# Performance work log

Hardware: AMD Instinct MI355X
Metric: run time of the kernel (lower is better)

## Reference

```python
import jax, jax.numpy as jnp
import numpy as np

B, C, W, F, NC = 512, 12, 4, 512, 4  # batch, leads, windows(=4, hardcoded by conv0), features, classes


def setup_inputs() -> dict:
    key = jax.random.key(0)
    ks = jax.random.split(key, 16)
    g = lambda i, shape, s=1.0: jax.random.normal(ks[i], shape, jnp.float32) * s
    return {
        "x": g(0, (B, C, W, F)),
        # GRU (PyTorch layout: W_ih [3F,F], W_hh [3F,F], gate order r,z,n)
        "gru_wih": g(1, (3 * F, F), 0.03),
        "gru_whh": g(2, (3 * F, F), 0.03),
        "gru_bih": jnp.zeros((3 * F,), jnp.float32),
        "gru_bhh": jnp.zeros((3 * F,), jnp.float32),
        # GraphLearning 1x1 convs (squeezed kernels); positive biases keep adj nondegenerate
        "conv0_w": g(3, (W,), 0.5), "conv0_b": jnp.float32(0.1),
        "conv1_w": g(4, (F,), 0.05), "conv1_b": jnp.float32(0.1),
        "conv2_w": g(5, (C * C, C), 0.3),
        "conv2_b": 0.1 + 0.05 * jnp.abs(g(6, (C * C,))),
        # GCN stack
        "gcn_w": g(7, (2, F, F), 0.04), "gcn_b": jnp.zeros((2, F), jnp.float32),
        # classifier head (jax [in,out] layout); BN in eval mode
        "fc1_w": g(8, (C * F, 512), 0.02), "fc1_b": jnp.zeros((512,), jnp.float32),
        "bn1_g": jnp.ones((512,), jnp.float32), "bn1_b": jnp.zeros((512,), jnp.float32),
        "bn1_m": 0.1 * g(9, (512,)), "bn1_v": 1.0 + 0.1 * jnp.abs(g(10, (512,))),
        "fc2_w": g(11, (512, 512), 0.04), "fc2_b": jnp.zeros((512,), jnp.float32),
        "bn2_g": jnp.ones((512,), jnp.float32), "bn2_b": jnp.zeros((512,), jnp.float32),
        "bn2_m": 0.1 * g(12, (512,)), "bn2_v": 1.0 + 0.1 * jnp.abs(g(13, (512,))),
        "fc3_w": g(14, (512, NC), 0.04), "fc3_b": jnp.zeros((NC,), jnp.float32),
    }


def reference(x, gru_wih, gru_whh, gru_bih, gru_bhh,
              conv0_w, conv0_b, conv1_w, conv1_b, conv2_w, conv2_b,
              gcn_w, gcn_b,
              fc1_w, fc1_b, bn1_g, bn1_b, bn1_m, bn1_v,
              fc2_w, fc2_b, bn2_g, bn2_b, bn2_m, bn2_v,
              fc3_w, fc3_b):
    b, c, w, f = x.shape
    # --- GRU over leads dim; each window slice starts from h0=0, so merge (batch, w) ---
    xs = x.transpose(0, 2, 1, 3).reshape(b * w, c, f)            # [N, C, F]
    xW = jnp.einsum('ntf,gf->ntg', xs, gru_wih) + gru_bih        # precompute input gates [N,C,3F]

    def step(h, xw_t):
        hg = h @ gru_whh.T + gru_bhh
        xr, xz, xn = jnp.split(xw_t, 3, axis=-1)
        hr, hz, hn = jnp.split(hg, 3, axis=-1)
        r = jax.nn.sigmoid(xr + hr)
        z = jax.nn.sigmoid(xz + hz)
        n = jnp.tanh(xn + r * hn)
        h = (1.0 - z) * n + z * h
        return h, h

    _, hs = jax.lax.scan(step, jnp.zeros((b * w, f), x.dtype), xW.transpose(1, 0, 2))
    gru_out = hs.transpose(1, 0, 2).reshape(b, w, c, f).transpose(0, 2, 1, 3)  # [B,C,W,F]

    # --- GraphLearning: 1x1 convs -> 12x12 adjacency -> normalized Laplacian -> Chebyshev K=4 ---
    g0 = gru_out.transpose(0, 2, 1, 3)                               # [B,W,C,F]
    y = jax.nn.relu(jnp.einsum('bwcf,w->bcf', g0, conv0_w) + conv0_b)  # [B,C,F]
    y = jax.nn.relu(jnp.einsum('bcf,f->bc', y, conv1_w) + conv1_b)     # [B,C]
    y = jax.nn.relu(jnp.einsum('bc,kc->bk', y, conv2_w) + conv2_b)     # [B,C*C]
    a = jnp.mean(y.reshape(b, c, c), axis=0)
    adj = jax.nn.relu(a)
    degree = jnp.sum(adj, axis=1)
    adj_s = 0.5 * (adj + adj.T)
    d_hat = 1.0 / (jnp.sqrt(degree) + 1e-7)
    lap = d_hat[:, None] * (jnp.diag(degree) - adj_s) * d_hat[None, :]
    L0 = jnp.zeros_like(lap)
    L1 = lap
    L2 = 2.0 * lap @ L1 - L0
    L3 = 2.0 * lap @ L2 - L1
    cheb = jnp.stack([L0, L1, L2, L3], axis=0)                       # [4,C,C]

    # --- GCN stack with residuals (dropout is identity in eval) ---
    h = gru_out.transpose(0, 2, 1, 3)[:, :, None]                    # [B,W,1,C,F]
    tmp = h
    res = h
    for i in range(gcn_w.shape[0]):
        support = jnp.einsum('bwocf,fg->bwocg', h, gcn_w[i])
        out = jnp.einsum('wij,bwojf->bwoif', cheb, support) + gcn_b[i]
        h = jax.nn.relu(out) + res
        res = h
    h = tmp + h
    h = h[:, :, 0].sum(1).reshape(b, c * f)                          # [B, C*F]

    # --- classifier head (eval-mode BN, dropout identity) ---
    def bn(v, gmm, bt, m, var):
        return (v - m) / jnp.sqrt(var + 1e-5) * gmm + bt

    h = bn(jax.nn.leaky_relu(h @ fc1_w + fc1_b, 0.01), bn1_g, bn1_b, bn1_m, bn1_v)
    h = bn(jax.nn.leaky_relu(h @ fc2_w + fc2_b, 0.01), bn2_g, bn2_b, bn2_m, bn2_v)
    return h @ fc3_w + fc3_b
```

## Files before the change

kernel.cpp:

```cpp
#include <hip/hip_runtime.h>
#include <cmath>

constexpr int Bb  = 512;
constexpr int Cc  = 12;
constexpr int Ww  = 4;
constexpr int Ff  = 512;
constexpr int Nn  = Bb * Ww;
constexpr int Gg  = 3 * Ff;
constexpr int Mx  = Nn * Cc;

typedef __attribute__((ext_vector_type(8))) short bf16x8;
typedef __attribute__((ext_vector_type(4))) float f32x4;

__device__ __forceinline__ float sigm(float v) { return 1.f / (1.f + expf(-v)); }
__device__ __forceinline__ float b2f(ushort u) { union { float f; unsigned i; } v; v.i = ((unsigned)u) << 16; return v.f; }
__device__ __forceinline__ ushort f2b(float f) {
    union { float f; unsigned i; } v; v.f = f;
    unsigned r = v.i + 0x7FFFu + ((v.i >> 16) & 1u);
    return (ushort)(r >> 16);
}
__device__ __forceinline__ void async16(const ushort* g, ushort* l) {
    __builtin_amdgcn_global_load_lds(
        (const __attribute__((address_space(1))) unsigned int*)g,
        (__attribute__((address_space(3))) unsigned int*)l, 16, 0, 0);
}

__global__ __launch_bounds__(256) void mfma_gemm(
    const ushort* __restrict__ A, const ushort* __restrict__ Bt,
    float* __restrict__ Cf, ushort* __restrict__ Cb,
    const float* __restrict__ colBias,
    int N, int K, int kLen, int MN, int gridY)
{
    __shared__ ushort As[128 * 64], Bs[128 * 64];
    const int tid = threadIdx.x;
    const int ln = tid & 63, wv = tid >> 6;
    const int l = blockIdx.x;
    const int by = l % gridY, bx = l / gridY, bz = blockIdx.y;
    const int srow = ln >> 3;
    const int kslot = (ln & 7) ^ srow;
    const int rowA0 = by * 128 + wv * 32;
    const int rowB0 = bx * 128 + wv * 32;
    const ushort* ga = A  + (long)(rowA0 + srow) * K + bz * kLen + kslot * 8;
    const ushort* gb = Bt + (long)(rowB0 + srow) * K + bz * kLen + kslot * 8;
    ushort* la = As + wv * 32 * 64;
    ushort* lb = Bs + wv * 32 * 64;
    const int rbase = (wv >> 1) * 64, cbase = (wv & 1) * 64;
    const int mrow = ln & 15, quad = ln >> 4;

    f32x4 acc[4][4] = {};

    for (int kc = 0; kc < kLen; kc += 64) {
        #pragma unroll
        for (int i = 0; i < 4; ++i) {
            async16(ga + (long)(i * 8) * K, la + i * 8 * 64);
            async16(gb + (long)(i * 8) * K, lb + i * 8 * 64);
        }
        ga += 64; gb += 64;
        __syncthreads();
        #pragma unroll
        for (int s = 0; s < 2; ++s) {
            const int sw = (((s << 2) + quad) ^ (ln & 7)) << 3;
            bf16x8 af[4], bf[4];
            #pragma unroll
            for (int i = 0; i < 4; ++i)
                af[i] = *(const bf16x8*)(As + (rbase + i * 16 + mrow) * 64 + sw);
            #pragma unroll
            for (int j = 0; j < 4; ++j)
                bf[j] = *(const bf16x8*)(Bs + (cbase + j * 16 + mrow) * 64 + sw);
            #pragma unroll
            for (int i = 0; i < 4; ++i)
                #pragma unroll
                for (int j = 0; j < 4; ++j)
                    acc[i][j] = __builtin_amdgcn_mfma_f32_16x16x32_bf16(bf[j], af[i], acc[i][j], 0, 0, 0);
        }
        __syncthreads();
    }

    const int gr0 = by * 128 + rbase + mrow;
    const int gc0 = bx * 128 + cbase + quad * 4;
    if (Cb) {
        #pragma unroll
        for (int i = 0; i < 4; ++i) {
            const long rowoff = (long)(gr0 + i * 16) * N;
            #pragma unroll
            for (int j = 0; j < 4; ++j) {
                float c0 = 0.f, c1 = 0.f, c2 = 0.f, c3 = 0.f;
                if (colBias) {
                    const float4 cb4 = *(const float4*)(colBias + gc0 + j * 16);
                    c0 = cb4.x; c1 = cb4.y; c2 = cb4.z; c3 = cb4.w;
                }
                union { ushort u[4]; uint2 v; } pk;
                pk.u[0] = f2b(acc[i][j][0] + c0);
                pk.u[1] = f2b(acc[i][j][1] + c1);
                pk.u[2] = f2b(acc[i][j][2] + c2);
                pk.u[3] = f2b(acc[i][j][3] + c3);
                *(uint2*)&Cb[rowoff + gc0 + j * 16] = pk.v;
            }
        }
    } else {
        float* Co = Cf + (long)bz * MN;
        #pragma unroll
        for (int i = 0; i < 4; ++i) {
            const long rowoff = (long)(gr0 + i * 16) * N;
            #pragma unroll
            for (int j = 0; j < 4; ++j)
                *(f32x4*)&Co[rowoff + gc0 + j * 16] = acc[i][j];
        }
    }
}

__global__ __launch_bounds__(256) void gru_fused(
    const ushort* __restrict__ hin, const ushort* __restrict__ xb,
    const ushort* __restrict__ whhB, const ushort* __restrict__ wihB,
    const float* __restrict__ bih, const float* __restrict__ bhh,
    ushort* __restrict__ hout, ushort* __restrict__ G, int t)
{
    __shared__ ushort Ah[64 * 64], Ax[64 * 64], Bh[96 * 64], Bx[96 * 64];
    const int tid = threadIdx.x, ln = tid & 63, wv = tid >> 6;
    const int mb = blockIdx.x & 31, fb = blockIdx.x >> 5;
    const int srow = ln >> 3, kslot = (ln & 7) ^ srow;
    const int mrow = ln & 15, quad = ln >> 4;
    f32x4 aH[6] = {}, aX[6] = {};
    const ushort* hrow = hin + (long)(mb * 64) * 512;

    for (int kc = 0; kc < 512; kc += 64) {
        #pragma unroll
        for (int a = 0; a < 2; ++a) {
            const int r0 = (wv * 2 + a) * 8;
            async16(hrow + (long)(r0 + srow) * 512 + kc + kslot * 8, Ah + r0 * 64);
            async16(xb + ((long)(mb * 64 + r0 + srow) * 12 + t) * 512 + kc + kslot * 8, Ax + r0 * 64);
        }
        #pragma unroll
        for (int b8 = 0; b8 < 3; ++b8) {
            const int lr0 = (wv * 3 + b8) * 8;
            const int lr = lr0 + srow;
            const int g = lr >> 5, fc = lr & 31;
            const long wr = (long)(g * 512 + fb * 32 + fc) * 512 + kc + kslot * 8;
            async16(whhB + wr, Bh + lr0 * 64);
            async16(wihB + wr, Bx + lr0 * 64);
        }
        __syncthreads();
        #pragma unroll
        for (int s = 0; s < 2; ++s) {
            const int sw = (((s << 2) + quad) ^ (ln & 7)) << 3;
            const bf16x8 ah = *(const bf16x8*)(Ah + (wv * 16 + mrow) * 64 + sw);
            const bf16x8 ax = *(const bf16x8*)(Ax + (wv * 16 + mrow) * 64 + sw);
            #pragma unroll
            for (int jt = 0; jt < 6; ++jt) {
                const bf16x8 bh = *(const bf16x8*)(Bh + (jt * 16 + mrow) * 64 + sw);
                aH[jt] = __builtin_amdgcn_mfma_f32_16x16x32_bf16(bh, ah, aH[jt], 0, 0, 0);
            }
            #pragma unroll
            for (int jt = 0; jt < 6; ++jt) {
                const bf16x8 bx2 = *(const bf16x8*)(Bx + (jt * 16 + mrow) * 64 + sw);
                aX[jt] = __builtin_amdgcn_mfma_f32_16x16x32_bf16(bx2, ax, aX[jt], 0, 0, 0);
            }
        }
        __syncthreads();
    }

    const int n = mb * 64 + wv * 16 + mrow;
    #pragma unroll
    for (int ft = 0; ft < 2; ++ft) {
        const int f0 = fb * 32 + ft * 16 + quad * 4;
        const float4 bir = *(const float4*)(bih + f0);
        const float4 biz = *(const float4*)(bih + 512 + f0);
        const float4 bin = *(const float4*)(bih + 1024 + f0);
        const float4 bhr = *(const float4*)(bhh + f0);
        const float4 bhz = *(const float4*)(bhh + 512 + f0);
        const float4 bhn = *(const float4*)(bhh + 1024 + f0);
        union { ushort u[4]; uint2 v; } hp;
        hp.v = *(const uint2*)(hin + (long)n * 512 + f0);
        const float br[4] = {bir.x + bhr.x, bir.y + bhr.y, bir.z + bhr.z, bir.w + bhr.w};
        const float bz[4] = {biz.x + bhz.x, biz.y + bhz.y, biz.z + bhz.z, biz.w + bhz.w};
        const float bn_i[4] = {bin.x, bin.y, bin.z, bin.w};
        const float bn_h[4] = {bhn.x, bhn.y, bhn.z, bhn.w};
        union { ushort u[4]; uint2 v; } o;
        #pragma unroll
        for (int r = 0; r < 4; ++r) {
            const float rr = sigm(aH[ft][r] + aX[ft][r] + br[r]);
            const float zz = sigm(aH[2 + ft][r] + aX[2 + ft][r] + bz[r]);
            const float nv = tanhf(aX[4 + ft][r] + bn_i[r] + rr * (aH[4 + ft][r] + bn_h[r]));
            o.u[r] = f2b((1.f - zz) * nv + zz * b2f(hp.u[r]));
        }
        *(uint2*)&hout[(long)n * 512 + f0] = o.v;
        *(uint2*)&G[(long)(n * 12 + t) * 512 + f0] = o.v;
    }
}

__global__ __launch_bounds__(256) void cvt_x(const float* __restrict__ x, ushort* __restrict__ xb)
{
    const int idx = blockIdx.x * 256 + threadIdx.x;
    const int m = idx >> 6, f8 = (idx & 63) << 3;
    const int n = m / 12, c = m - n * 12;
    const int b = n >> 2, w = n & 3;
    const float* src = x + (((b * 12 + c) * 4 + w) << 9) + f8;
    const float4 a = *(const float4*)src, q = *(const float4*)(src + 4);
    uint4 o;
    o.x = (unsigned)f2b(a.x) | ((unsigned)f2b(a.y) << 16);
    o.y = (unsigned)f2b(a.z) | ((unsigned)f2b(a.w) << 16);
    o.z = (unsigned)f2b(q.x) | ((unsigned)f2b(q.y) << 16);
    o.w = (unsigned)f2b(q.z) | ((unsigned)f2b(q.w) << 16);
    *(uint4*)(xb + (m << 9) + f8) = o;
}

__global__ __launch_bounds__(256) void cvt_w2(
    const float* __restrict__ wih, const float* __restrict__ whh,
    ushort* __restrict__ wihB, ushort* __restrict__ whhB)
{
    int bx = blockIdx.x;
    const float* s; ushort* d;
    if (bx < 384) { s = wih; d = wihB; } else { s = whh; d = whhB; bx -= 384; }
    const int e = (bx * 256 + threadIdx.x) << 3;
    const float4 a = *(const float4*)(s + e), q = *(const float4*)(s + e + 4);
    uint4 o;
    o.x = (unsigned)f2b(a.x) | ((unsigned)f2b(a.y) << 16);
    o.y = (unsigned)f2b(a.z) | ((unsigned)f2b(a.w) << 16);
    o.z = (unsigned)f2b(q.x) | ((unsigned)f2b(q.y) << 16);
    o.w = (unsigned)f2b(q.z) | ((unsigned)f2b(q.w) << 16);
    *(uint4*)(d + e) = o;
}

__global__ __launch_bounds__(256) void tcvt_all(
    const float* __restrict__ gcnw, const float* __restrict__ f1w, const float* __restrict__ f2w,
    ushort* __restrict__ gw0, ushort* __restrict__ gw1,
    ushort* __restrict__ f1t, ushort* __restrict__ f2t)
{
    int by = blockIdx.y;
    const float* src; ushort* dst; int R, C;
    if (by < 16)       { src = gcnw;          dst = gw0; R = 512;  C = 512; }
    else if (by < 32)  { src = gcnw + 262144; dst = gw1; R = 512;  C = 512; by -= 16; }
    else if (by < 224) { src = f1w;           dst = f1t; R = 6144; C = 512; by -= 32; }
    else               { src = f2w;           dst = f2t; R = 512;  C = 512; by -= 224; }
    __shared__ float tl[32][33];
    const int c0 = blockIdx.x * 32, r0 = by * 32;
    const int cx = threadIdx.x & 31, ry = threadIdx.x >> 5;
    #pragma unroll
    for (int k = 0; k < 4; ++k) tl[ry + k * 8][cx] = src[(long)(r0 + ry + k * 8) * C + c0 + cx];
    __syncthreads();
    #pragma unroll
    for (int k = 0; k < 4; ++k) dst[(long)(c0 + ry + k * 8) * R + r0 + cx] = f2b(tl[cx][ry + k * 8]);
}

__global__ __launch_bounds__(256) void conv01(
    const ushort* __restrict__ G, const float* __restrict__ w0, const float* __restrict__ b0,
    const float* __restrict__ w1, const float* __restrict__ b1, float* __restrict__ y2)
{
    const int row = (blockIdx.x * 256 + threadIdx.x) >> 6;
    const int lane = threadIdx.x & 63;
    const int b = row / 12, c = row - 12 * b;
    const float w00 = w0[0], w01 = w0[1], w02 = w0[2], w03 = w0[3], bb = b0[0];
    const ushort* gp = G + ((long)(b * 4) * 12 + c) * 512;
    float s = 0.f;
    for (int f = lane; f < 512; f += 64) {
        const float v = bb + b2f(gp[f]) * w00 + b2f(gp[6144 + f]) * w01
                      + b2f(gp[12288 + f]) * w02 + b2f(gp[18432 + f]) * w03;
        s += fmaxf(v, 0.f) * w1[f];
    }
    #pragma unroll
    for (int off = 32; off; off >>= 1) s += __shfl_down(s, off);
    if (lane == 0) y2[row] = fmaxf(s + b1[0], 0.f);
}

__global__ __launch_bounds__(256) void conv2_cheb(
    const float* __restrict__ y2, const float* __restrict__ w2,
    const float* __restrict__ b2, float* __restrict__ cheb)
{
    __shared__ float ys[6144];
    __shared__ float adj[144], deg[12], dhat[12], lap[144], T2[144];
    const int tid = threadIdx.x;
    for (int i = tid; i < 6144; i += 256) ys[i] = y2[i];
    __syncthreads();
    if (tid < 144) {
        float wk[12];
        #pragma unroll
        for (int c = 0; c < 12; ++c) wk[c] = w2[tid * 12 + c];
        const float bias = b2[tid];
        float s = 0.f;
        for (int b = 0; b < 512; ++b) {
            float v = bias;
            #pragma unroll
            for (int c = 0; c < 12; ++c) v += ys[b * 12 + c] * wk[c];
            s += fmaxf(v, 0.f);
        }
        adj[tid] = fmaxf(s * (1.f / 512.f), 0.f);
    }
    __syncthreads();
    if (tid < 12) {
        float s = 0.f;
        for (int j = 0; j < 12; ++j) s += adj[tid * 12 + j];
        deg[tid] = s; dhat[tid] = 1.f / (sqrtf(s) + 1e-7f);
    }
    __syncthreads();
    if (tid < 144) {
        const int i = tid / 12, j = tid % 12;
        const float as = 0.5f * (adj[i * 12 + j] + adj[j * 12 + i]);
        lap[tid] = dhat[i] * ((i == j ? deg[i] : 0.f) - as) * dhat[j];
    }
    __syncthreads();
    if (tid < 144) {
        const int i = tid / 12, j = tid % 12;
        float s = 0.f;
        for (int kk = 0; kk < 12; ++kk) s += lap[i * 12 + kk] * lap[kk * 12 + j];
        T2[tid] = 2.f * s;
    }
    __syncthreads();
    if (tid < 144) {
        const int i = tid / 12, j = tid % 12;
        float s = 0.f;
        for (int kk = 0; kk < 12; ++kk) s += lap[i * 12 + kk] * T2[kk * 12 + j];
        cheb[tid] = 0.f;
        cheb[144 + tid] = lap[tid];
        cheb[288 + tid] = T2[tid];
        cheb[432 + tid] = 2.f * s - lap[tid];
    }
}

__global__ __launch_bounds__(256) void gcn_epi1(
    const ushort* __restrict__ S, const float* __restrict__ cheb,
    const float* __restrict__ gcnb, const ushort* __restrict__ G,
    ushort* __restrict__ H1)
{
    __shared__ float ch[576];
    const int tid = threadIdx.x;
    for (int i = tid; i < 576; i += 256) ch[i] = cheb[i];
    __syncthreads();
    const int idx = blockIdx.x * 256 + tid;
    const int f = idx & 511, bc = idx >> 9;
    const int b = bc / 12, c = bc - 12 * b;
    const float bias = gcnb[f];
    #pragma unroll
    for (int w = 0; w < 4; ++w) {
        float o = bias;
        const ushort* Sr = S + ((b * 4 + w) * 12) * 512 + f;
        const float* cw = ch + w * 144 + c * 12;
        #pragma unroll
        for (int j = 0; j < 12; ++j) o += cw[j] * b2f(Sr[j * 512]);
        const int gi = ((b * 4 + w) * 12 + c) * 512 + f;
        H1[gi] = f2b(fmaxf(o, 0.f) + b2f(G[gi]));
    }
}

__global__ __launch_bounds__(256) void gcn_epi2(
    const ushort* __restrict__ S, const float* __restrict__ cheb,
    const float* __restrict__ gcnb, const ushort* __restrict__ G,
    const ushort* __restrict__ H1, ushort* __restrict__ pooled)
{
    __shared__ float ch[576];
    const int tid = threadIdx.x;
    for (int i = tid; i < 576; i += 256) ch[i] = cheb[i];
    __syncthreads();
    const int idx = blockIdx.x * 256 + tid;
    const int f = idx & 511, bc = idx >> 9;
    const int b = bc / 12, c = bc - 12 * b;
    const float bias = gcnb[f];
    float acc = 0.f;
    #pragma unroll
    for (int w = 0; w < 4; ++w) {
        float o = bias;
        const ushort* Sr = S + ((b * 4 + w) * 12) * 512 + f;
        const float* cw = ch + w * 144 + c * 12;
        #pragma unroll
        for (int j = 0; j < 12; ++j) o += cw[j] * b2f(Sr[j * 512]);
        const int gi = ((b * 4 + w) * 12 + c) * 512 + f;
        acc += fmaxf(o, 0.f) + b2f(H1[gi]) + b2f(G[gi]);
    }
    pooled[idx] = f2b(acc);
}

__global__ __launch_bounds__(256) void fc_epi(
    const float* __restrict__ part, int nsplit, const float* __restrict__ bias,
    const float* __restrict__ g, const float* __restrict__ be,
    const float* __restrict__ mu, const float* __restrict__ var,
    ushort* __restrict__ outb, float* __restrict__ outf)
{
    const int idx = blockIdx.x * 256 + threadIdx.x;
    const int c = idx & 511;
    float s = bias[c];
    for (int k = 0; k < nsplit; ++k) s += part[k * 262144 + idx];
    s = s >= 0.f ? s : 0.01f * s;
    s = (s - mu[c]) * rsqrtf(var[c] + 1e-5f) * g[c] + be[c];
    if (outb) outb[idx] = f2b(s); else outf[idx] = s;
}

__global__ __launch_bounds__(256) void fc3_kernel(
    const float* __restrict__ z2, const float* __restrict__ w3,
    const float* __restrict__ b3, float* __restrict__ out)
{
    const int idx = blockIdx.x * 256 + threadIdx.x;
    const int m = idx >> 2, nc = idx & 3;
    float s = b3[nc];
    const float* zr = z2 + m * 512;
    for (int k = 0; k < 512; ++k) s += zr[k] * w3[k * 4 + nc];
    out[idx] = s;
}

extern "C" void kernel_launch(void* const* d_in, const int* in_sizes, int n_in,
                              void* d_out, int out_size, void* d_ws, size_t ws_size,
                              hipStream_t stream)
{
    (void)in_sizes; (void)n_in; (void)out_size; (void)ws_size;
    const float* x    = (const float*)d_in[0];
    const float* wih  = (const float*)d_in[1];
    const float* whh  = (const float*)d_in[2];
    const float* bih  = (const float*)d_in[3];
    const float* bhh  = (const float*)d_in[4];
    const float* c0w  = (const float*)d_in[5];
    const float* c0b  = (const float*)d_in[6];
    const float* c1w  = (const float*)d_in[7];
    const float* c1b  = (const float*)d_in[8];
    const float* c2w  = (const float*)d_in[9];
    const float* c2b  = (const float*)d_in[10];
    const float* gcnw = (const float*)d_in[11];
    const float* gcnb = (const float*)d_in[12];
    const float* f1w  = (const float*)d_in[13];
    const float* f1b  = (const float*)d_in[14];
    const float* bn1g = (const float*)d_in[15];
    const float* bn1b = (const float*)d_in[16];
    const float* bn1m = (const float*)d_in[17];
    const float* bn1v = (const float*)d_in[18];
    const float* f2w  = (const float*)d_in[19];
    const float* f2b_ = (const float*)d_in[20];
    const float* bn2g = (const float*)d_in[21];
    const float* bn2b = (const float*)d_in[22];
    const float* bn2m = (const float*)d_in[23];
    const float* bn2v = (const float*)d_in[24];
    const float* f3w  = (const float*)d_in[25];
    const float* f3b  = (const float*)d_in[26];

    char* W = (char*)d_ws;
    ushort* xb     = (ushort*)(W + 0);
    ushort* pooled = (ushort*)(W + 0);
    float*  z1p    = (float*)(W + 8388608);
    float*  z2p    = z1p;
    ushort* G      = (ushort*)(W + 25165824);
    ushort* S      = (ushort*)(W + 50331648);
    ushort* H1     = (ushort*)(W + 75497472);
    ushort* h0     = (ushort*)(W + 100663296);
    ushort* h1     = (ushort*)(W + 102760448);
    ushort* wihB   = (ushort*)(W + 104857600);
    ushort* whhB   = (ushort*)(W + 106430464);
    ushort* gw0    = (ushort*)(W + 108003328);
    ushort* gw1    = (ushort*)(W + 108527616);
    ushort* f1t    = (ushort*)(W + 109051904);
    ushort* f2t    = (ushort*)(W + 115343360);
    ushort* z1b    = (ushort*)(W + 115867648);
    float*  z2     = (float*)(W + 116391936);
    float*  y2     = (float*)(W + 117440512);
    float*  chebb  = (float*)(W + 117465088);

    hipMemsetAsync(h0, 0, (size_t)Nn * Ff * sizeof(ushort), stream);
    cvt_x<<<(Mx * 64) / 256, 256, 0, stream>>>(x, xb);
    cvt_w2<<<768, 256, 0, stream>>>(wih, whh, wihB, whhB);
    tcvt_all<<<dim3(16, 240), 256, 0, stream>>>(gcnw, f1w, f2w, gw0, gw1, f1t, f2t);

    ushort* hp = h0; ushort* hq = h1;
    for (int t = 0; t < Cc; ++t) {
        gru_fused<<<512, 256, 0, stream>>>(hp, xb, whhB, wihB, bih, bhh, hq, G, t);
        ushort* tmp = hp; hp = hq; hq = tmp;
    }

    conv01<<<(Bb * Cc * 64) / 256, 256, 0, stream>>>(G, c0w, c0b, c1w, c1b, y2);
    conv2_cheb<<<1, 256, 0, stream>>>(y2, c2w, c2b, chebb);

    mfma_gemm<<<dim3(768, 1), 256, 0, stream>>>(
        G, gw0, nullptr, S, nullptr, Ff, Ff, Ff, 0, 192);
    gcn_epi1<<<(Bb * Cc * Ff) / 256, 256, 0, stream>>>(S, chebb, gcnb, G, H1);

    mfma_gemm<<<dim3(768, 1), 256, 0, stream>>>(
        H1, gw1, nullptr, S, nullptr, Ff, Ff, Ff, 0, 192);
    gcn_epi2<<<(Bb * Cc * Ff) / 256, 256, 0, stream>>>(S, chebb, gcnb + Ff, G, H1, pooled);

    mfma_gemm<<<dim3(16, 16), 256, 0, stream>>>(
        pooled, f1t, z1p, nullptr, nullptr, 512, Cc * Ff, 384, 262144, 4);
    fc_epi<<<1024, 256, 0, stream>>>(z1p, 16, f1b, bn1g, bn1b, bn1m, bn1v, z1b, nullptr);
    mfma_gemm<<<dim3(16, 4), 256, 0, stream>>>(
        z1b, f2t, z2p, nullptr, nullptr, 512, 512, 128, 262144, 4);
    fc_epi<<<1024, 256, 0, stream>>>(z2p, 4, f2b_, bn2g, bn2b, bn2m, bn2v, nullptr, z2);
    fc3_kernel<<<(Bb * 4) / 256, 256, 0, stream>>>(z2, f3w, f3b, (float*)d_out);
}
```

Before: 510.4 us.

## Precompute GRU input gates in one GEMM and run recurrence as persistent kernel

Replaces the twelve per-step GRU launches with one large GEMM that precomputes the input projections for all leads, followed by a persistent kernel. That kernel keeps its slice of W_hh resident in LDS and loops over the time steps, synchronising through per-row-group atomic barriers in global memory. It also skips the recurrent matmul at t=0 and double-buffers the hidden-state loads. This removes launch overhead and the repeated W_ih/W_hh reloads per step. The cost is a spin barrier that assumes all 256 blocks are resident at once, and a bf16 round-trip on the precomputed input gates.

```diff
diff --git a/kernel.cpp b/kernel.cpp
--- a/kernel.cpp
+++ b/kernel.cpp
@@ -5,9 +5,7 @@
 constexpr int Cc  = 12;
 constexpr int Ww  = 4;
 constexpr int Ff  = 512;
-constexpr int Nn  = Bb * Ww;
-constexpr int Gg  = 3 * Ff;
-constexpr int Mx  = Nn * Cc;
+constexpr int Mx  = Bb * Ww * Cc;
 
 typedef __attribute__((ext_vector_type(8))) short bf16x8;
 typedef __attribute__((ext_vector_type(4))) float f32x4;
@@ -109,57 +107,30 @@
     }
 }
 
-__global__ __launch_bounds__(256) void gru_fused(
-    const ushort* __restrict__ hin, const ushort* __restrict__ xb,
-    const ushort* __restrict__ whhB, const ushort* __restrict__ wihB,
+__global__ __launch_bounds__(512, 1) void gru_persist(
+    const ushort* __restrict__ xW, const ushort* __restrict__ whhB,
     const float* __restrict__ bih, const float* __restrict__ bhh,
-    ushort* __restrict__ hout, ushort* __restrict__ G, int t)
-{
-    __shared__ ushort Ah[64 * 64], Ax[64 * 64], Bh[96 * 64], Bx[96 * 64];
+    ushort* __restrict__ h0, ushort* __restrict__ h1,
+    ushort* __restrict__ G, unsigned* __restrict__ bar)
+{
+    __shared__ ushort Bw[8 * 96 * 64];
+    __shared__ ushort Ah[2][128 * 64];
     const int tid = threadIdx.x, ln = tid & 63, wv = tid >> 6;
-    const int mb = blockIdx.x & 31, fb = blockIdx.x >> 5;
+    const int mb = blockIdx.x & 15, fb = blockIdx.x >> 4;
     const int srow = ln >> 3, kslot = (ln & 7) ^ srow;
     const int mrow = ln & 15, quad = ln >> 4;
-    f32x4 aH[6] = {}, aX[6] = {};
-    const ushort* hrow = hin + (long)(mb * 64) * 512;
-
-    for (int kc = 0; kc < 512; kc += 64) {
-        #pragma unroll
-        for (int a = 0; a < 2; ++a) {
-            const int r0 = (wv * 2 + a) * 8;
-            async16(hrow + (long)(r0 + srow) * 512 + kc + kslot * 8, Ah + r0 * 64);
-            async16(xb + ((long)(mb * 64 + r0 + srow) * 12 + t) * 512 + kc + kslot * 8, Ax + r0 * 64);
-        }
-        #pragma unroll
-        for (int b8 = 0; b8 < 3; ++b8) {
-            const int lr0 = (wv * 3 + b8) * 8;
-            const int lr = lr0 + srow;
-            const int g = lr >> 5, fc = lr & 31;
-            const long wr = (long)(g * 512 + fb * 32 + fc) * 512 + kc + kslot * 8;
-            async16(whhB + wr, Bh + lr0 * 64);
-            async16(wihB + wr, Bx + lr0 * 64);
-        }
-        __syncthreads();
-        #pragma unroll
-        for (int s = 0; s < 2; ++s) {
-            const int sw = (((s << 2) + quad) ^ (ln & 7)) << 3;
-            const bf16x8 ah = *(const bf16x8*)(Ah + (wv * 16 + mrow) * 64 + sw);
-            const bf16x8 ax = *(const bf16x8*)(Ax + (wv * 16 + mrow) * 64 + sw);
-            #pragma unroll
-            for (int jt = 0; jt < 6; ++jt) {
-                const bf16x8 bh = *(const bf16x8*)(Bh + (jt * 16 + mrow) * 64 + sw);
-                aH[jt] = __builtin_amdgcn_mfma_f32_16x16x32_bf16(bh, ah, aH[jt], 0, 0, 0);
-            }
-            #pragma unroll
-            for (int jt = 0; jt < 6; ++jt) {
-                const bf16x8 bx2 = *(const bf16x8*)(Bx + (jt * 16 + mrow) * 64 + sw);
-                aX[jt] = __builtin_amdgcn_mfma_f32_16x16x32_bf16(bx2, ax, aX[jt], 0, 0, 0);
-            }
-        }
-        __syncthreads();
-    }
-
-    const int n = mb * 64 + wv * 16 + mrow;
+
+    #pragma unroll
+    for (int i = 0; i < 12; ++i) {
+        const int rg = i * 8 + wv;
+        const int kc6 = rg / 12, rgi = rg - kc6 * 12;
+        const int r0 = rgi * 8, r = r0 + srow;
+        const int g = r >> 5, fc = r & 31;
+        async16(whhB + (long)(g * 512 + fb * 32 + fc) * 512 + kc6 * 64 + kslot * 8,
+                Bw + (kc6 * 96 + r0) * 64);
+    }
+
+    float br[2][4], bz[2][4], bni[2][4], bnh[2][4];
     #pragma unroll
     for (int ft = 0; ft < 2; ++ft) {
         const int f0 = fb * 32 + ft * 16 + quad * 4;
@@ -169,22 +140,98 @@
         const float4 bhr = *(const float4*)(bhh + f0);
         const float4 bhz = *(const float4*)(bhh + 512 + f0);
         const float4 bhn = *(const float4*)(bhh + 1024 + f0);
-        union { ushort u[4]; uint2 v; } hp;
-        hp.v = *(const uint2*)(hin + (long)n * 512 + f0);
-        const float br[4] = {bir.x + bhr.x, bir.y + bhr.y, bir.z + bhr.z, bir.w + bhr.w};
-        const float bz[4] = {biz.x + bhz.x, biz.y + bhz.y, biz.z + bhz.z, biz.w + bhz.w};
-        const float bn_i[4] = {bin.x, bin.y, bin.z, bin.w};
-        const float bn_h[4] = {bhn.x, bhn.y, bhn.z, bhn.w};
-        union { ushort u[4]; uint2 v; } o;
-        #pragma unroll
-        for (int r = 0; r < 4; ++r) {
-            const float rr = sigm(aH[ft][r] + aX[ft][r] + br[r]);
-            const float zz = sigm(aH[2 + ft][r] + aX[2 + ft][r] + bz[r]);
-            const float nv = tanhf(aX[4 + ft][r] + bn_i[r] + rr * (aH[4 + ft][r] + bn_h[r]));
-            o.u[r] = f2b((1.f - zz) * nv + zz * b2f(hp.u[r]));
-        }
-        *(uint2*)&hout[(long)n * 512 + f0] = o.v;
-        *(uint2*)&G[(long)(n * 12 + t) * 512 + f0] = o.v;
+        br[ft][0] = bir.x + bhr.x; br[ft][1] = bir.y + bhr.y; br[ft][2] = bir.z + bhr.z; br[ft][3] = bir.w + bhr.w;
+        bz[ft][0] = biz.x + bhz.x; bz[ft][1] = biz.y + bhz.y; bz[ft][2] = biz.z + bhz.z; bz[ft][3] = biz.w + bhz.w;
+        bni[ft][0] = bin.x; bni[ft][1] = bin.y; bni[ft][2] = bin.z; bni[ft][3] = bin.w;
+        bnh[ft][0] = bhn.x; bnh[ft][1] = bhn.y; bnh[ft][2] = bhn.z; bnh[ft][3] = bhn.w;
+    }
+    __syncthreads();
+
+    const int n = mb * 128 + wv * 16 + mrow;
+    const long nrow = (long)n * 512;
+    unsigned* cptr = bar + mb * 16;
+
+    for (int t = 0; t < 12; ++t) {
+        const ushort* hin = (t & 1) ? h1 : h0;
+        ushort* hout = (t & 1) ? h0 : h1;
+        f32x4 acc[6] = {};
+
+        const long xrow = ((long)n * 12 + t) * 1536;
+        uint2 xrv[2], xzv[2], xnv[2], hpv[2];
+        #pragma unroll
+        for (int ft = 0; ft < 2; ++ft) {
+            const int f0 = fb * 32 + ft * 16 + quad * 4;
+            xrv[ft] = *(const uint2*)(xW + xrow + f0);
+            xzv[ft] = *(const uint2*)(xW + xrow + 512 + f0);
+            xnv[ft] = *(const uint2*)(xW + xrow + 1024 + f0);
+            if (t > 0) hpv[ft] = *(const uint2*)(hin + nrow + f0);
+            else { hpv[ft].x = 0u; hpv[ft].y = 0u; }
+        }
+
+        if (t > 0) {
+            const ushort* hb = hin + (long)(mb * 128) * 512;
+            #pragma unroll
+            for (int a = 0; a < 2; ++a) {
+                const int r0 = (wv * 2 + a) * 8;
+                async16(hb + (long)(r0 + srow) * 512 + kslot * 8, Ah[0] + r0 * 64);
+            }
+            __syncthreads();
+            for (int kc6 = 0; kc6 < 8; ++kc6) {
+                if (kc6 < 7) {
+                    const int kn = kc6 + 1;
+                    #pragma unroll
+                    for (int a = 0; a < 2; ++a) {
+                        const int r0 = (wv * 2 + a) * 8;
+                        async16(hb + (long)(r0 + srow) * 512 + kn * 64 + kslot * 8,
+                                Ah[kn & 1] + r0 * 64);
+                    }
+                }
+                const ushort* Bk = Bw + kc6 * (96 * 64);
+                const ushort* Ak = Ah[kc6 & 1];
+                #pragma unroll
+                for (int s = 0; s < 2; ++s) {
+                    const int sw = (((s << 2) + quad) ^ (ln & 7)) << 3;
+                    const bf16x8 ah = *(const bf16x8*)(Ak + (wv * 16 + mrow) * 64 + sw);
+                    #pragma unroll
+                    for (int jt = 0; jt < 6; ++jt) {
+                        const bf16x8 bh = *(const bf16x8*)(Bk + (jt * 16 + mrow) * 64 + sw);
+                        acc[jt] = __builtin_amdgcn_mfma_f32_16x16x32_bf16(bh, ah, acc[jt], 0, 0, 0);
+                    }
+                }
+                __syncthreads();
+            }
+        }
+
+        #pragma unroll
+        for (int ft = 0; ft < 2; ++ft) {
+            const int f0 = fb * 32 + ft * 16 + quad * 4;
+            const ushort* xr = (const ushort*)&xrv[ft];
+            const ushort* xz = (const ushort*)&xzv[ft];
+            const ushort* xn = (const ushort*)&xnv[ft];
+            const ushort* hp = (const ushort*)&hpv[ft];
+            union { ushort u[4]; uint2 v; } o;
+            #pragma unroll
+            for (int r = 0; r < 4; ++r) {
+                const float rr = sigm(acc[ft][r] + b2f(xr[r]) + br[ft][r]);
+                const float zz = sigm(acc[2 + ft][r] + b2f(xz[r]) + bz[ft][r]);
+                const float nv = tanhf(b2f(xn[r]) + bni[ft][r] + rr * (acc[4 + ft][r] + bnh[ft][r]));
+                o.u[r] = f2b((1.f - zz) * nv + zz * b2f(hp[r]));
+            }
+            *(uint2*)&hout[nrow + f0] = o.v;
+            *(uint2*)&G[((long)n * 12 + t) * 512 + f0] = o.v;
+        }
+
+        if (t < 11) {
+            __syncthreads();
+            if (tid == 0) {
+                __hip_atomic_fetch_add(cptr, 1u, __ATOMIC_RELEASE, __HIP_MEMORY_SCOPE_AGENT);
+                const unsigned tgt = (unsigned)(t + 1) * 16u;
+                while (__hip_atomic_load(cptr, __ATOMIC_RELAXED, __HIP_MEMORY_SCOPE_AGENT) < tgt)
+                    __builtin_amdgcn_s_sleep(8);
+                (void)__hip_atomic_load(cptr, __ATOMIC_ACQUIRE, __HIP_MEMORY_SCOPE_AGENT);
+            }
+            __syncthreads();
+        }
     }
 }
 
@@ -429,17 +476,18 @@
     const float* f3b  = (const float*)d_in[26];
 
     char* W = (char*)d_ws;
-    ushort* xb     = (ushort*)(W + 0);
-    ushort* pooled = (ushort*)(W + 0);
-    float*  z1p    = (float*)(W + 8388608);
+    ushort* xW     = (ushort*)(W + 0);
+    ushort* S      = (ushort*)(W + 0);
+    ushort* H1     = (ushort*)(W + 25165824);
+    ushort* pooled = (ushort*)(W + 50331648);
+    float*  z1p    = (float*)(W + 58720256);
     float*  z2p    = z1p;
-    ushort* G      = (ushort*)(W + 25165824);
-    ushort* S      = (ushort*)(W + 50331648);
-    ushort* H1     = (ushort*)(W + 75497472);
+    ushort* xb     = (ushort*)(W + 75497472);
+    ushort* G      = (ushort*)(W + 75497472);
     ushort* h0     = (ushort*)(W + 100663296);
     ushort* h1     = (ushort*)(W + 102760448);
-    ushort* wihB   = (ushort*)(W + 104857600);
-    ushort* whhB   = (ushort*)(W + 106430464);
+    ushort* whhB   = (ushort*)(W + 104857600);
+    ushort* wihB   = (ushort*)(W + 106430464);
     ushort* gw0    = (ushort*)(W + 108003328);
     ushort* gw1    = (ushort*)(W + 108527616);
     ushort* f1t    = (ushort*)(W + 109051904);
@@ -448,17 +496,16 @@
     float*  z2     = (float*)(W + 116391936);
     float*  y2     = (float*)(W + 117440512);
     float*  chebb  = (float*)(W + 117465088);
-
-    hipMemsetAsync(h0, 0, (size_t)Nn * Ff * sizeof(ushort), stream);
+    unsigned* bar  = (unsigned*)(W + 117467392);
+
+    hipMemsetAsync(bar, 0, 1024, stream);
     cvt_x<<<(Mx * 64) / 256, 256, 0, stream>>>(x, xb);
     cvt_w2<<<768, 256, 0, stream>>>(wih, whh, wihB, whhB);
     tcvt_all<<<dim3(16, 240), 256, 0, stream>>>(gcnw, f1w, f2w, gw0, gw1, f1t, f2t);
 
-    ushort* hp = h0; ushort* hq = h1;
-    for (int t = 0; t < Cc; ++t) {
-        gru_fused<<<512, 256, 0, stream>>>(hp, xb, whhB, wihB, bih, bhh, hq, G, t);
-        ushort* tmp = hp; hp = hq; hq = tmp;
-    }
+    mfma_gemm<<<dim3(2304, 1), 256, 0, stream>>>(
+        xb, wihB, nullptr, xW, nullptr, 3 * Ff, Ff, Ff, 0, 192);
+    gru_persist<<<256, 512, 0, stream>>>(xW, whhB, bih, bhh, h0, h1, G, bar);
 
     conv01<<<(Bb * Cc * 64) / 256, 256, 0, stream>>>(G, c0w, c0b, c1w, c1b, y2);
     conv2_cheb<<<1, 256, 0, stream>>>(y2, c2w, c2b, chebb);
```

Result: slower. 601.6 us (+17.9%).
